# Kernel tuning notes

Hardware: AMD Instinct MI355X
Metric: run time of the kernel (lower is better)

Reference implementation:

```python
import jax, jax.numpy as jnp
from jax import lax
import numpy as np

DN = ('NCHW', 'OIHW', 'NCHW')


def _conv(x, w, b, stride, pad):
    y = lax.conv_general_dilated(x, w, (stride, stride), [(pad, pad), (pad, pad)],
                                 dimension_numbers=DN)
    return y + b[None, :, None, None]


def _conv_t(x, w, b):
    # torch ConvTranspose2d(k=4, stride=2, padding=1) equivalent:
    # lhs_dilation=2, effective padding k-1-p = 2 on each side -> output 2H x 2W
    y = lax.conv_general_dilated(x, w, (1, 1), [(2, 2), (2, 2)],
                                 lhs_dilation=(2, 2), dimension_numbers=DN)
    return y + b[None, :, None, None]


def setup_inputs() -> dict:
    key = jax.random.key(0)
    ks = jax.random.split(key, 16)
    D, K = 8, 512  # latent_dim, codebook_size

    def w(k, shape, fan_in):
        return jax.random.normal(k, shape, jnp.float32) * (1.0 / np.sqrt(fan_in))

    inp = {
        'x': jax.random.uniform(ks[0], (32, 3, 256, 256), jnp.float32),
        # encoder
        'enc_w1': w(ks[1], (32, 3, 4, 4), 3 * 16), 'enc_b1': jnp.zeros((32,), jnp.float32),
        'enc_w2': w(ks[2], (64, 32, 4, 4), 32 * 16), 'enc_b2': jnp.zeros((64,), jnp.float32),
        'enc_w3': w(ks[3], (D, 64, 1, 1), 64), 'enc_b3': jnp.zeros((D,), jnp.float32),
        # codebook, uniform(-1/K, 1/K) as in torch init
        'codebook': jax.random.uniform(ks[4], (K, D), jnp.float32, -1.0 / K, 1.0 / K),
        # decoder
        'dec_w1': w(ks[5], (64, D, 3, 3), D * 9), 'dec_b1': jnp.zeros((64,), jnp.float32),
        'dect_w1': w(ks[6], (64, 64, 4, 4), 64 * 16), 'dect_b1': jnp.zeros((64,), jnp.float32),
        'dect_w2': w(ks[7], (32, 64, 4, 4), 64 * 16), 'dect_b2': jnp.zeros((32,), jnp.float32),
        'dec_w2': w(ks[8], (3, 32, 3, 3), 32 * 9), 'dec_b2': jnp.zeros((3,), jnp.float32),
    }
    return inp


def reference(x, enc_w1, enc_b1, enc_w2, enc_b2, enc_w3, enc_b3, codebook,
              dec_w1, dec_b1, dect_w1, dect_b1, dect_w2, dect_b2, dec_w2, dec_b2):
    commitment_cost = 0.25
    B = x.shape[0]
    D = codebook.shape[1]

    # encoder
    h = jax.nn.relu(_conv(x, enc_w1, enc_b1, 2, 1))
    h = jax.nn.relu(_conv(h, enc_w2, enc_b2, 2, 1))
    z = _conv(h, enc_w3, enc_b3, 1, 0)                      # [B, D, H/4, W/4]

    # VQ: pairwise squared distances, argmin, gather
    z_flat = z.transpose(0, 2, 3, 1).reshape(-1, D)          # [N, D] in NHWC order
    distances = (jnp.sum(z_flat ** 2, axis=1, keepdims=True)
                 + jnp.sum(codebook ** 2, axis=1)
                 - 2.0 * z_flat @ codebook.T)                 # [N, K]
    encoding_indices = jnp.argmin(distances, axis=1)          # [N]
    # NOTE: faithful to original bug - reshaped directly into NCHW without permute
    z_q = codebook[encoding_indices].reshape(z.shape)

    commitment_loss = jnp.mean((z - lax.stop_gradient(z_q)) ** 2)
    codebook_loss = jnp.mean((z_q - lax.stop_gradient(z)) ** 2)
    vq_loss = codebook_loss + commitment_cost * commitment_loss

    # straight-through estimator
    z_q = z + lax.stop_gradient(z_q - z)

    # decoder
    h = jax.nn.relu(_conv(z_q, dec_w1, dec_b1, 1, 1))
    h = jax.nn.relu(_conv_t(h, dect_w1, dect_b1))
    h = jax.nn.relu(_conv_t(h, dect_w2, dect_b2))
    x_recon = jax.nn.sigmoid(_conv(h, dec_w2, dec_b2, 1, 1))

    return x_recon, vq_loss, encoding_indices.reshape(B, -1)
```

## Files before the change

### kernel.cpp

```cpp
#include <hip/hip_runtime.h>
#include <hip/hip_bf16.h>
#include <math.h>


__device__ __forceinline__ int rfl(int v) { return __builtin_amdgcn_readfirstlane(v); }

typedef __attribute__((ext_vector_type(8))) short s8v;
typedef __attribute__((ext_vector_type(4))) float f4v;

__device__ __forceinline__ ushort f2bf(float f) {
    __hip_bfloat16 h = __float2bfloat16(f);
    return *(ushort*)&h;
}

__global__ __launch_bounds__(256) void k_conv1(const float* __restrict__ x, const float* __restrict__ w,
                                               const float* __restrict__ bias, float* __restrict__ out) {
    int t = blockIdx.x * 256 + threadIdx.x;
    int ow  = t & 127;
    int oh0 = ((t >> 7) & 31) * 4;
    int co0 = rfl((t >> 12) & 3) * 8;
    int b   = rfl(t >> 14);
    float acc[4][8] = {};
    for (int ci = 0; ci < 3; ci++) {
        const float* xp = x + (b * 3 + ci) * 65536;
        const float* wp = w + (co0 * 3 + ci) * 16;
        #pragma unroll
        for (int r = 0; r < 10; r++) {
            int ih = oh0 * 2 - 1 + r;
            bool rok = (ih >= 0) && (ih < 256);
            int ihc = rok ? ih : 0;
            float v[4];
            #pragma unroll
            for (int c = 0; c < 4; c++) {
                int iw = ow * 2 - 1 + c;
                bool ok = rok && (iw >= 0) && (iw < 256);
                int iwc = iw < 0 ? 0 : (iw > 255 ? 255 : iw);
                float vv = xp[ihc * 256 + iwc];
                v[c] = ok ? vv : 0.f;
            }
            #pragma unroll
            for (int o = 0; o < 4; o++) {
                int kh = r - 2 * o;
                if (kh >= 0 && kh < 4) {
                    #pragma unroll
                    for (int cc = 0; cc < 8; cc++) {
                        const float* wc = wp + cc * 48 + kh * 4;
                        acc[o][cc] = __builtin_fmaf(v[0], wc[0], acc[o][cc]);
                        acc[o][cc] = __builtin_fmaf(v[1], wc[1], acc[o][cc]);
                        acc[o][cc] = __builtin_fmaf(v[2], wc[2], acc[o][cc]);
                        acc[o][cc] = __builtin_fmaf(v[3], wc[3], acc[o][cc]);
                    }
                }
            }
        }
    }
    #pragma unroll
    for (int cc = 0; cc < 8; cc++) {
        float bv = bias[co0 + cc];
        #pragma unroll
        for (int o = 0; o < 4; o++) {
            float v = acc[o][cc] + bv;
            out[((b * 32 + co0 + cc) * 128 + oh0 + o) * 128 + ow] = v > 0.f ? v : 0.f;
        }
    }
}

__global__ __launch_bounds__(256) void k_conv2t(const float* __restrict__ h1, const float* __restrict__ w,
                                                const float* __restrict__ bias, float* __restrict__ out) {
    __shared__ float P[16][18][2][10];
    int bx = blockIdx.x;
    int b  = bx >> 6;
    int ty = (bx >> 3) & 7, tx = bx & 7;
    int oh0 = ty * 8, ow0 = tx * 8;
    int tid = threadIdx.x;
    int lane = tid & 63;
    int dy = lane >> 3, dx = lane & 7;
    int co_base = rfl(tid >> 6) * 16;
    int oh = oh0 + dy, ow = ow0 + dx;
    float s00 = 0.f, s01 = 0.f, s02 = 0.f, s03 = 0.f;
    float s10 = 0.f, s11 = 0.f, s12 = 0.f, s13 = 0.f;
    float s20 = 0.f, s21 = 0.f, s22 = 0.f, s23 = 0.f;
    float s30 = 0.f, s31 = 0.f, s32 = 0.f, s33 = 0.f;

    #pragma unroll
    for (int pass = 0; pass < 2; pass++) {
        int cib = pass * 16;
        __syncthreads();
        for (int i = tid; i < 16 * 18 * 18; i += 256) {
            int cl = i / 324, rem = i - cl * 324;
            int r = rem / 18, c = rem - r * 18;
            int ih = oh0 * 2 - 1 + r, iw = ow0 * 2 - 1 + c;
            float v = 0.f;
            if (ih >= 0 && ih < 128 && iw >= 0 && iw < 128)
                v = h1[(b * 32 + cib + cl) * 16384 + ih * 128 + iw];
            P[cl][r][c & 1][c >> 1] = v;
        }
        __syncthreads();
        #pragma unroll
        for (int cc = 0; cc < 4; cc++) {
            int co0 = co_base + cc * 4;
            float a0 = (cc == 0) ? s00 : (cc == 1) ? s10 : (cc == 2) ? s20 : s30;
            float a1 = (cc == 0) ? s01 : (cc == 1) ? s11 : (cc == 2) ? s21 : s31;
            float a2 = (cc == 0) ? s02 : (cc == 1) ? s12 : (cc == 2) ? s22 : s32;
            float a3 = (cc == 0) ? s03 : (cc == 1) ? s13 : (cc == 2) ? s23 : s33;
            for (int cl = 0; cl < 16; cl++) {
                const float* wp0 = w + ((co0 + 0) * 32 + cib + cl) * 16;
                const float* wp1 = w + ((co0 + 1) * 32 + cib + cl) * 16;
                const float* wp2 = w + ((co0 + 2) * 32 + cib + cl) * 16;
                const float* wp3 = w + ((co0 + 3) * 32 + cib + cl) * 16;
                #pragma unroll
                for (int kh = 0; kh < 4; kh++) {
                    int r = 2 * dy + kh;
                    float v0 = P[cl][r][0][dx];
                    float v1 = P[cl][r][1][dx];
                    float v2 = P[cl][r][0][dx + 1];
                    float v3 = P[cl][r][1][dx + 1];
                    a0 = __builtin_fmaf(v0, wp0[kh*4+0], a0); a0 = __builtin_fmaf(v1, wp0[kh*4+1], a0);
                    a0 = __builtin_fmaf(v2, wp0[kh*4+2], a0); a0 = __builtin_fmaf(v3, wp0[kh*4+3], a0);
                    a1 = __builtin_fmaf(v0, wp1[kh*4+0], a1); a1 = __builtin_fmaf(v1, wp1[kh*4+1], a1);
                    a1 = __builtin_fmaf(v2, wp1[kh*4+2], a1); a1 = __builtin_fmaf(v3, wp1[kh*4+3], a1);
                    a2 = __builtin_fmaf(v0, wp2[kh*4+0], a2); a2 = __builtin_fmaf(v1, wp2[kh*4+1], a2);
                    a2 = __builtin_fmaf(v2, wp2[kh*4+2], a2); a2 = __builtin_fmaf(v3, wp2[kh*4+3], a2);
                    a3 = __builtin_fmaf(v0, wp3[kh*4+0], a3); a3 = __builtin_fmaf(v1, wp3[kh*4+1], a3);
                    a3 = __builtin_fmaf(v2, wp3[kh*4+2], a3); a3 = __builtin_fmaf(v3, wp3[kh*4+3], a3);
                }
            }
            if (cc == 0)      { s00 = a0; s01 = a1; s02 = a2; s03 = a3; }
            else if (cc == 1) { s10 = a0; s11 = a1; s12 = a2; s13 = a3; }
            else if (cc == 2) { s20 = a0; s21 = a1; s22 = a2; s23 = a3; }
            else              { s30 = a0; s31 = a1; s32 = a2; s33 = a3; }
        }
    }
    float r0, r1, r2, r3;
    #pragma unroll
    for (int cc = 0; cc < 4; cc++) {
        int co0 = co_base + cc * 4;
        if (cc == 0)      { r0 = s00; r1 = s01; r2 = s02; r3 = s03; }
        else if (cc == 1) { r0 = s10; r1 = s11; r2 = s12; r3 = s13; }
        else if (cc == 2) { r0 = s20; r1 = s21; r2 = s22; r3 = s23; }
        else              { r0 = s30; r1 = s31; r2 = s32; r3 = s33; }
        float v0 = r0 + bias[co0 + 0], v1 = r1 + bias[co0 + 1];
        float v2 = r2 + bias[co0 + 2], v3 = r3 + bias[co0 + 3];
        out[((b * 64 + co0 + 0) * 64 + oh) * 64 + ow] = v0 > 0.f ? v0 : 0.f;
        out[((b * 64 + co0 + 1) * 64 + oh) * 64 + ow] = v1 > 0.f ? v1 : 0.f;
        out[((b * 64 + co0 + 2) * 64 + oh) * 64 + ow] = v2 > 0.f ? v2 : 0.f;
        out[((b * 64 + co0 + 3) * 64 + oh) * 64 + ow] = v3 > 0.f ? v3 : 0.f;
    }
}

__global__ __launch_bounds__(256) void k_conv3(const float* __restrict__ h2, const float* __restrict__ w,
                                               const float* __restrict__ bias, float* __restrict__ zf) {
    __shared__ float wl[8][64];
    __shared__ float bl[8];
    int tid = threadIdx.x;
    for (int i = tid; i < 512; i += 256) wl[i >> 6][i & 63] = w[i];
    if (tid < 8) bl[tid] = bias[tid];
    __syncthreads();
    int t = blockIdx.x * 256 + tid;
    int b = t >> 12, hw = t & 4095;
    float acc[8];
    for (int d = 0; d < 8; d++) acc[d] = 0.f;
    for (int ci = 0; ci < 64; ci++) {
        float v = h2[(b * 64 + ci) * 4096 + hw];
        for (int d = 0; d < 8; d++) acc[d] = __builtin_fmaf(v, wl[d][ci], acc[d]);
    }
    for (int d = 0; d < 8; d++)
        zf[(b * 8 + d) * 4096 + hw] = acc[d] + bl[d];
}

__global__ __launch_bounds__(256) void k_vq(const float* __restrict__ zf, const float* __restrict__ cb,
                                            int* __restrict__ idx, float* __restrict__ out_idx) {
    __shared__ float cbs[512][8];
    __shared__ float c2s[512];
    int tid = threadIdx.x;
    for (int i = tid; i < 4096; i += 256) cbs[i >> 3][i & 7] = cb[i];
    __syncthreads();
    for (int k = tid; k < 512; k += 256) {
        float s = 0.f;
        for (int d = 0; d < 8; d++) {
            float c = cbs[k][d];
            s = s + __fmul_rn(c, c);
        }
        c2s[k] = s;
    }
    __syncthreads();
    int n = blockIdx.x * 256 + tid;
    int b = n >> 12, hw = n & 4095;
    float zv[8], s1 = 0.f;
    for (int d = 0; d < 8; d++) {
        float z = zf[(b * 8 + d) * 4096 + hw];
        zv[d] = z;
        s1 = s1 + __fmul_rn(z, z);
    }
    float best = 3.4e38f; int bi = 0;
    for (int k = 0; k < 512; k++) {
        float dot = 0.f;
        for (int d = 0; d < 8; d++) dot = __builtin_fmaf(zv[d], cbs[k][d], dot);
        float a = s1 + c2s[k];
        float dist = a - __fmul_rn(2.0f, dot);
        if (dist < best) { best = dist; bi = k; }
    }
    idx[n] = bi;
    out_idx[n] = (float)bi;
}

__global__ __launch_bounds__(256) void k_zq(const int* __restrict__ idx, const float* __restrict__ cb,
                                            const float* __restrict__ zf, float* __restrict__ zq,
                                            double* __restrict__ partial) {
    __shared__ double red[256];
    int t = blockIdx.x * 256 + threadIdx.x;
    float q = cb[idx[t >> 3] * 8 + (t & 7)];
    zq[t] = q;
    double d = (double)zf[t] - (double)q;
    red[threadIdx.x] = d * d;
    __syncthreads();
    for (int s = 128; s > 0; s >>= 1) {
        if (threadIdx.x < s) red[threadIdx.x] += red[threadIdx.x + s];
        __syncthreads();
    }
    if (threadIdx.x == 0) partial[blockIdx.x] = red[0];
}

__global__ __launch_bounds__(256) void k_loss_fin(const double* __restrict__ partial, float* __restrict__ out_loss) {
    __shared__ double red[256];
    double s = 0.0;
    for (int i = threadIdx.x; i < 4096; i += 256) s += partial[i];
    red[threadIdx.x] = s;
    __syncthreads();
    for (int st = 128; st > 0; st >>= 1) {
        if (threadIdx.x < st) red[threadIdx.x] += red[threadIdx.x + st];
        __syncthreads();
    }
    if (threadIdx.x == 0)
        out_loss[0] = (float)(1.25 * red[0] / 1048576.0);
}

__global__ __launch_bounds__(256) void k_dec1(const float* __restrict__ zq, const float* __restrict__ w,
                                              const float* __restrict__ bias, float* __restrict__ out) {
    int t = blockIdx.x * 256 + threadIdx.x;
    int ow  = t & 63;
    int oh0 = ((t >> 6) & 15) * 4;
    int co0 = rfl((t >> 10) & 7) * 8;
    int b   = rfl(t >> 13);
    float acc[4][8] = {};
    for (int ci = 0; ci < 8; ci++) {
        const float* ip = zq + (b * 8 + ci) * 4096;
        const float* wp = w + (co0 * 8 + ci) * 9;
        #pragma unroll
        for (int r = 0; r < 6; r++) {
            int ih = oh0 - 1 + r;
            bool rok = (ih >= 0) && (ih < 64);
            int ihc = rok ? ih : 0;
            float v[3];
            #pragma unroll
            for (int c = 0; c < 3; c++) {
                int iw = ow - 1 + c;
                bool ok = rok && (iw >= 0) && (iw < 64);
                int iwc = iw < 0 ? 0 : (iw > 63 ? 63 : iw);
                float vv = ip[ihc * 64 + iwc];
                v[c] = ok ? vv : 0.f;
            }
            #pragma unroll
            for (int o = 0; o < 4; o++) {
                int kh = r - o;
                if (kh >= 0 && kh < 3) {
                    #pragma unroll
                    for (int cc = 0; cc < 8; cc++) {
                        const float* wc = wp + cc * 72 + kh * 3;
                        acc[o][cc] = __builtin_fmaf(v[0], wc[0], acc[o][cc]);
                        acc[o][cc] = __builtin_fmaf(v[1], wc[1], acc[o][cc]);
                        acc[o][cc] = __builtin_fmaf(v[2], wc[2], acc[o][cc]);
                    }
                }
            }
        }
    }
    #pragma unroll
    for (int cc = 0; cc < 8; cc++) {
        float bv = bias[co0 + cc];
        #pragma unroll
        for (int o = 0; o < 4; o++) {
            float v = acc[o][cc] + bv;
            out[((b * 64 + co0 + cc) * 64 + oh0 + o) * 64 + ow] = v > 0.f ? v : 0.f;
        }
    }
}

template <int CI, int CO>
__global__ __launch_bounds__(256) void k_wprep(const float* __restrict__ w, ushort* __restrict__ Wf) {
    constexpr int NT = CO / 16;
    int t = blockIdx.x * 256 + threadIdx.x;
    if (t >= 4 * NT * 8 * 64) return;
    int lane = t & 63;
    int kt = (t >> 6) & 7;
    int nt = (t >> 9) % NT;
    int q  = t / (512 * NT);
    int py = q >> 1, px = q & 1;
    int n = nt * 16 + (lane & 15);
    int cb = (kt & 1) * 32 + (lane >> 4) * 8;
    int tap = kt >> 1, dy = tap >> 1, dx = tap & 1;
    #pragma unroll
    for (int jj = 0; jj < 8; jj++) {
        int ci = cb + jj;
        float v = w[((n * CI + ci) * 4 + (py + 2 * dy)) * 4 + (px + 2 * dx)];
        Wf[(((q * NT + nt) * 8 + kt) * 64 + lane) * 8 + jj] = f2bf(v);
    }
}

template <int CI, int CO, int HIN>
__global__ __launch_bounds__(256) void k_dect_mfma(const float* __restrict__ in, const ushort* __restrict__ Wf,
                                                   const float* __restrict__ bias, float* __restrict__ out) {
    constexpr int NT = CO / 16;
    constexpr int TILES = HIN / 16;
    constexpr int HOUT = 2 * HIN;
    __shared__ alignas(16) ushort L[18 * 18 * 72];
    int blk = blockIdx.x;
    int b = blk / (TILES * TILES);
    int tile = blk - b * (TILES * TILES);
    int i0 = (tile / TILES) * 16, j0 = (tile % TILES) * 16;
    const float* ip = in + (size_t)b * CI * HIN * HIN;
    for (int e = threadIdx.x; e < 18 * 18 * CI; e += 256) {
        int ci = e / 324; int rem = e - ci * 324;
        int row = rem / 18; int col = rem - row * 18;
        int ih = i0 - 1 + row, iw = j0 - 1 + col;
        float v = 0.f;
        if (ih >= 0 && ih < HIN && iw >= 0 && iw < HIN)
            v = ip[(size_t)ci * (HIN * HIN) + ih * HIN + iw];
        L[(row * 18 + col) * 72 + ci] = f2bf(v);
    }
    __syncthreads();
    int wv = threadIdx.x >> 6;
    int lane = threadIdx.x & 63;
    int py = wv >> 1, px = wv & 1;
    int m = lane & 15, quad = lane >> 4;
    const ushort* wq = Wf + (size_t)wv * NT * 8 * 64 * 8;
    for (int il = 0; il < 16; il++) {
        s8v a[8];
        #pragma unroll
        for (int kt = 0; kt < 8; kt++) {
            int tap = kt >> 1, dy = tap >> 1, dx = tap & 1;
            int r = il + py + dy, cl = m + px + dx;
            a[kt] = *(s8v*)&L[(r * 18 + cl) * 72 + (kt & 1) * 32 + quad * 8];
        }
        #pragma unroll
        for (int nt = 0; nt < NT; nt++) {
            f4v acc = {0.f, 0.f, 0.f, 0.f};
            #pragma unroll
            for (int kt = 0; kt < 8; kt++) {
                s8v bf = *(const s8v*)&wq[((nt * 8 + kt) * 64 + lane) * 8];
                acc = __builtin_amdgcn_mfma_f32_16x16x32_bf16(a[kt], bf, acc, 0, 0, 0);
            }
            int co = nt * 16 + m;
            float bv = bias[co];
            int y = 2 * (i0 + il) + py;
            #pragma unroll
            for (int reg = 0; reg < 4; reg++) {
                int jD = j0 + quad * 4 + reg;
                int xx = 2 * jD + px;
                float v = acc[reg] + bv;
                out[((size_t)(b * CO + co) * HOUT + y) * HOUT + xx] = v > 0.f ? v : 0.f;
            }
        }
    }
}

__global__ __launch_bounds__(256) void k_dec2(const float* __restrict__ in, const float* __restrict__ w,
                                              const float* __restrict__ bias, float* __restrict__ out) {
    int t = blockIdx.x * 256 + threadIdx.x;
    int x  = t & 255;
    int y0 = ((t >> 8) & 63) * 4;
    int b  = rfl(t >> 14);
    float acc[4][3] = {};
    for (int ci = 0; ci < 32; ci++) {
        const float* ip = in + (size_t)(b * 32 + ci) * 65536;
        const float* wp = w + ci * 9;
        #pragma unroll
        for (int rr = 0; rr < 6; rr++) {
            int ih = y0 - 1 + rr;
            bool rok = (ih >= 0) && (ih < 256);
            int ihc = rok ? ih : 0;
            float v[3];
            #pragma unroll
            for (int c = 0; c < 3; c++) {
                int iw = x - 1 + c;
                bool ok = rok && (iw >= 0) && (iw < 256);
                int iwc = iw < 0 ? 0 : (iw > 255 ? 255 : iw);
                float vv = ip[ihc * 256 + iwc];
                v[c] = ok ? vv : 0.f;
            }
            #pragma unroll
            for (int o = 0; o < 4; o++) {
                int kh = rr - o;
                if (kh >= 0 && kh < 3) {
                    #pragma unroll
                    for (int co = 0; co < 3; co++) {
                        const float* wc = wp + co * 288 + kh * 3;
                        acc[o][co] = __builtin_fmaf(v[0], wc[0], acc[o][co]);
                        acc[o][co] = __builtin_fmaf(v[1], wc[1], acc[o][co]);
                        acc[o][co] = __builtin_fmaf(v[2], wc[2], acc[o][co]);
                    }
                }
            }
        }
    }
    #pragma unroll
    for (int co = 0; co < 3; co++) {
        float bv = bias[co];
        #pragma unroll
        for (int o = 0; o < 4; o++) {
            float v = acc[o][co] + bv;
            out[((size_t)(b * 3 + co) * 256 + y0 + o) * 256 + x] = 1.0f / (1.0f + expf(-v));
        }
    }
}

extern "C" void kernel_launch(void* const* d_in, const int* in_sizes, int n_in,
                              void* d_out, int out_size, void* d_ws, size_t ws_size,
                              hipStream_t stream) {
    const float* x    = (const float*)d_in[0];
    const float* ew1  = (const float*)d_in[1];
    const float* eb1  = (const float*)d_in[2];
    const float* ew2  = (const float*)d_in[3];
    const float* eb2  = (const float*)d_in[4];
    const float* ew3  = (const float*)d_in[5];
    const float* eb3  = (const float*)d_in[6];
    const float* cb   = (const float*)d_in[7];
    const float* dw1  = (const float*)d_in[8];
    const float* db1  = (const float*)d_in[9];
    const float* dtw1 = (const float*)d_in[10];
    const float* dtb1 = (const float*)d_in[11];
    const float* dtw2 = (const float*)d_in[12];
    const float* dtb2 = (const float*)d_in[13];
    const float* dw2  = (const float*)d_in[14];
    const float* db2  = (const float*)d_in[15];

    char* ws = (char*)d_ws;
    float*  z32  = (float*) (ws);
    float*  zq   = (float*) (ws + 4194304);
    int*    idx  = (int*)   (ws + 8388608);
    double* part = (double*)(ws + 8912896);
    ushort* Wf1  = (ushort*)(ws + 8945664);
    ushort* Wf2  = (ushort*)(ws + 9076736);
    char* region = ws + 9142272;

    size_t fixed = 9142272;
    size_t avail = (ws_size > fixed) ? ws_size - fixed : 0;
    int ce = 32, cd = 32;
    while (ce > 1 && (size_t)ce * 3145728ull > avail) ce >>= 1;
    while (cd > 1 && (size_t)cd * 13631488ull > avail) cd >>= 1;

    float* h1c = (float*)region;
    float* h2c = (float*)(region + (size_t)ce * 2097152ull);
    float* d3c = (float*) region;
    float* d4c = (float*) (region + (size_t)cd * 1048576ull);
    float* d5c = (float*) (region + (size_t)cd * 5242880ull);

    float* out      = (float*)d_out;
    float* out_loss = out + 6291456;
    float* out_idx  = out + 6291457;

    for (int c = 0; c < 32 / ce; c++) {
        const float* xc = x + (size_t)c * ce * 196608ull;
        k_conv1<<<ce * 64, 256, 0, stream>>>(xc, ew1, eb1, h1c);
        k_conv2t<<<ce * 64, 256, 0, stream>>>(h1c, ew2, eb2, h2c);
        k_conv3<<<ce * 16,  256, 0, stream>>>(h2c, ew3, eb3, z32 + (size_t)c * ce * 32768ull);
    }

    k_vq<<<512, 256, 0, stream>>>(z32, cb, idx, out_idx);
    k_zq<<<4096, 256, 0, stream>>>(idx, cb, z32, zq, part);
    k_loss_fin<<<1, 256, 0, stream>>>(part, out_loss);

    k_wprep<64, 64><<<32, 256, 0, stream>>>(dtw1, Wf1);
    k_wprep<64, 32><<<16, 256, 0, stream>>>(dtw2, Wf2);

    for (int c = 0; c < 32 / cd; c++) {
        const float* zqc = zq + (size_t)c * cd * 32768ull;
        float* outc = out + (size_t)c * cd * 196608ull;
        k_dec1<<<cd * 32, 256, 0, stream>>>(zqc, dw1, db1, d3c);
        k_dect_mfma<64, 64, 64 ><<<cd * 16, 256, 0, stream>>>(d3c, Wf1, dtb1, d4c);
        k_dect_mfma<64, 32, 128><<<cd * 64, 256, 0, stream>>>(d4c, Wf2, dtb2, d5c);
        k_dec2<<<cd * 64, 256, 0, stream>>>(d5c, dw2, db2, outc);
    }
}
```

Baseline: 982.7 us.

## Store decoder intermediates in bf16, halve deconv tiles, and register-prefetch conv2 inputs

Decoder intermediates (dec1, both transposed-conv outputs) are now stored as bf16 instead of fp32. This halves their global memory traffic and removes the per-element conversion at LDS staging in the MFMA kernels. The MFMA deconv tiles shrink from 16x16 to 8x16, doubling the block count and cutting LDS use. The encoder conv2 kernel now processes 8 input channels per pass and prefetches the next slab into registers so global loads overlap compute. The cost is extra precision loss from rounding intermediates to bf16, plus more barriers and passes in conv2.

```diff
diff --git a/kernel.cpp b/kernel.cpp
--- a/kernel.cpp
+++ b/kernel.cpp
@@ -11,6 +11,9 @@
 __device__ __forceinline__ ushort f2bf(float f) {
     __hip_bfloat16 h = __float2bfloat16(f);
     return *(ushort*)&h;
+}
+__device__ __forceinline__ float bf2f(ushort u) {
+    return __uint_as_float(((unsigned int)u) << 16);
 }
 
 __global__ __launch_bounds__(256) void k_conv1(const float* __restrict__ x, const float* __restrict__ w,
@@ -67,7 +70,7 @@
 
 __global__ __launch_bounds__(256) void k_conv2t(const float* __restrict__ h1, const float* __restrict__ w,
                                                 const float* __restrict__ bias, float* __restrict__ out) {
-    __shared__ float P[16][18][2][10];
+    __shared__ float P[8][18][2][10];
     int bx = blockIdx.x;
     int b  = bx >> 6;
     int ty = (bx >> 3) & 7, tx = bx & 7;
@@ -81,21 +84,49 @@
     float s10 = 0.f, s11 = 0.f, s12 = 0.f, s13 = 0.f;
     float s20 = 0.f, s21 = 0.f, s22 = 0.f, s23 = 0.f;
     float s30 = 0.f, s31 = 0.f, s32 = 0.f, s33 = 0.f;
-
+    float pf[11];
     #pragma unroll
-    for (int pass = 0; pass < 2; pass++) {
-        int cib = pass * 16;
-        __syncthreads();
-        for (int i = tid; i < 16 * 18 * 18; i += 256) {
+    for (int k = 0; k < 11; k++) {
+        int i = tid + (k << 8);
+        float v = 0.f;
+        if (i < 2592) {
             int cl = i / 324, rem = i - cl * 324;
             int r = rem / 18, c = rem - r * 18;
             int ih = oh0 * 2 - 1 + r, iw = ow0 * 2 - 1 + c;
-            float v = 0.f;
             if (ih >= 0 && ih < 128 && iw >= 0 && iw < 128)
-                v = h1[(b * 32 + cib + cl) * 16384 + ih * 128 + iw];
-            P[cl][r][c & 1][c >> 1] = v;
-        }
+                v = h1[(b * 32 + cl) * 16384 + ih * 128 + iw];
+        }
+        pf[k] = v;
+    }
+    for (int pass = 0; pass < 4; pass++) {
         __syncthreads();
+        #pragma unroll
+        for (int k = 0; k < 11; k++) {
+            int i = tid + (k << 8);
+            if (i < 2592) {
+                int cl = i / 324, rem = i - cl * 324;
+                int r = rem / 18, c = rem - r * 18;
+                P[cl][r][c & 1][c >> 1] = pf[k];
+            }
+        }
+        __syncthreads();
+        if (pass < 3) {
+            int cib = (pass + 1) * 8;
+            #pragma unroll
+            for (int k = 0; k < 11; k++) {
+                int i = tid + (k << 8);
+                float v = 0.f;
+                if (i < 2592) {
+                    int cl = i / 324, rem = i - cl * 324;
+                    int r = rem / 18, c = rem - r * 18;
+                    int ih = oh0 * 2 - 1 + r, iw = ow0 * 2 - 1 + c;
+                    if (ih >= 0 && ih < 128 && iw >= 0 && iw < 128)
+                        v = h1[(b * 32 + cib + cl) * 16384 + ih * 128 + iw];
+                }
+                pf[k] = v;
+            }
+        }
+        int cib = pass * 8;
         #pragma unroll
         for (int cc = 0; cc < 4; cc++) {
             int co0 = co_base + cc * 4;
@@ -103,7 +134,7 @@
             float a1 = (cc == 0) ? s01 : (cc == 1) ? s11 : (cc == 2) ? s21 : s31;
             float a2 = (cc == 0) ? s02 : (cc == 1) ? s12 : (cc == 2) ? s22 : s32;
             float a3 = (cc == 0) ? s03 : (cc == 1) ? s13 : (cc == 2) ? s23 : s33;
-            for (int cl = 0; cl < 16; cl++) {
+            for (int cl = 0; cl < 8; cl++) {
                 const float* wp0 = w + ((co0 + 0) * 32 + cib + cl) * 16;
                 const float* wp1 = w + ((co0 + 1) * 32 + cib + cl) * 16;
                 const float* wp2 = w + ((co0 + 2) * 32 + cib + cl) * 16;
@@ -236,7 +267,7 @@
 }
 
 __global__ __launch_bounds__(256) void k_dec1(const float* __restrict__ zq, const float* __restrict__ w,
-                                              const float* __restrict__ bias, float* __restrict__ out) {
+                                              const float* __restrict__ bias, ushort* __restrict__ out) {
     int t = blockIdx.x * 256 + threadIdx.x;
     int ow  = t & 63;
     int oh0 = ((t >> 6) & 15) * 4;
@@ -281,7 +312,7 @@
         #pragma unroll
         for (int o = 0; o < 4; o++) {
             float v = acc[o][cc] + bv;
-            out[((b * 64 + co0 + cc) * 64 + oh0 + o) * 64 + ow] = v > 0.f ? v : 0.f;
+            out[((b * 64 + co0 + cc) * 64 + oh0 + o) * 64 + ow] = f2bf(v > 0.f ? v : 0.f);
         }
     }
 }
@@ -308,25 +339,27 @@
 }
 
 template <int CI, int CO, int HIN>
-__global__ __launch_bounds__(256) void k_dect_mfma(const float* __restrict__ in, const ushort* __restrict__ Wf,
-                                                   const float* __restrict__ bias, float* __restrict__ out) {
+__global__ __launch_bounds__(256) void k_dect_mfma(const ushort* __restrict__ in, const ushort* __restrict__ Wf,
+                                                   const float* __restrict__ bias, ushort* __restrict__ out) {
     constexpr int NT = CO / 16;
-    constexpr int TILES = HIN / 16;
+    constexpr int TX = HIN / 16;
+    constexpr int TY = HIN / 8;
     constexpr int HOUT = 2 * HIN;
-    __shared__ alignas(16) ushort L[18 * 18 * 72];
+    __shared__ alignas(16) ushort L[10 * 18 * 72];
     int blk = blockIdx.x;
-    int b = blk / (TILES * TILES);
-    int tile = blk - b * (TILES * TILES);
-    int i0 = (tile / TILES) * 16, j0 = (tile % TILES) * 16;
-    const float* ip = in + (size_t)b * CI * HIN * HIN;
-    for (int e = threadIdx.x; e < 18 * 18 * CI; e += 256) {
-        int ci = e / 324; int rem = e - ci * 324;
+    int b = blk / (TY * TX);
+    int tile = blk - b * (TY * TX);
+    int tyy = tile / TX, txx = tile - tyy * TX;
+    int i0 = tyy * 8, j0 = txx * 16;
+    const ushort* ip = in + (size_t)b * CI * HIN * HIN;
+    for (int e = threadIdx.x; e < 10 * 18 * CI; e += 256) {
+        int ci = e / 180; int rem = e - ci * 180;
         int row = rem / 18; int col = rem - row * 18;
         int ih = i0 - 1 + row, iw = j0 - 1 + col;
-        float v = 0.f;
+        ushort v = 0;
         if (ih >= 0 && ih < HIN && iw >= 0 && iw < HIN)
             v = ip[(size_t)ci * (HIN * HIN) + ih * HIN + iw];
-        L[(row * 18 + col) * 72 + ci] = f2bf(v);
+        L[(row * 18 + col) * 72 + ci] = v;
     }
     __syncthreads();
     int wv = threadIdx.x >> 6;
@@ -334,7 +367,7 @@
     int py = wv >> 1, px = wv & 1;
     int m = lane & 15, quad = lane >> 4;
     const ushort* wq = Wf + (size_t)wv * NT * 8 * 64 * 8;
-    for (int il = 0; il < 16; il++) {
+    for (int il = 0; il < 8; il++) {
         s8v a[8];
         #pragma unroll
         for (int kt = 0; kt < 8; kt++) {
@@ -358,13 +391,13 @@
                 int jD = j0 + quad * 4 + reg;
                 int xx = 2 * jD + px;
                 float v = acc[reg] + bv;
-                out[((size_t)(b * CO + co) * HOUT + y) * HOUT + xx] = v > 0.f ? v : 0.f;
-            }
-        }
-    }
-}
-
-__global__ __launch_bounds__(256) void k_dec2(const float* __restrict__ in, const float* __restrict__ w,
+                out[((size_t)(b * CO + co) * HOUT + y) * HOUT + xx] = f2bf(v > 0.f ? v : 0.f);
+            }
+        }
+    }
+}
+
+__global__ __launch_bounds__(256) void k_dec2(const ushort* __restrict__ in, const float* __restrict__ w,
                                               const float* __restrict__ bias, float* __restrict__ out) {
     int t = blockIdx.x * 256 + threadIdx.x;
     int x  = t & 255;
@@ -372,7 +405,7 @@
     int b  = rfl(t >> 14);
     float acc[4][3] = {};
     for (int ci = 0; ci < 32; ci++) {
-        const float* ip = in + (size_t)(b * 32 + ci) * 65536;
+        const ushort* ip = in + (size_t)(b * 32 + ci) * 65536;
         const float* wp = w + ci * 9;
         #pragma unroll
         for (int rr = 0; rr < 6; rr++) {
@@ -385,7 +418,7 @@
                 int iw = x - 1 + c;
                 bool ok = rok && (iw >= 0) && (iw < 256);
                 int iwc = iw < 0 ? 0 : (iw > 255 ? 255 : iw);
-                float vv = ip[ihc * 256 + iwc];
+                float vv = bf2f(ip[ihc * 256 + iwc]);
                 v[c] = ok ? vv : 0.f;
             }
             #pragma unroll
@@ -447,13 +480,13 @@
     size_t avail = (ws_size > fixed) ? ws_size - fixed : 0;
     int ce = 32, cd = 32;
     while (ce > 1 && (size_t)ce * 3145728ull > avail) ce >>= 1;
-    while (cd > 1 && (size_t)cd * 13631488ull > avail) cd >>= 1;
-
-    float* h1c = (float*)region;
-    float* h2c = (float*)(region + (size_t)ce * 2097152ull);
-    float* d3c = (float*) region;
-    float* d4c = (float*) (region + (size_t)cd * 1048576ull);
-    float* d5c = (float*) (region + (size_t)cd * 5242880ull);
+    while (cd > 1 && (size_t)cd * 6815744ull > avail) cd >>= 1;
+
+    float*  h1c = (float*)region;
+    float*  h2c = (float*)(region + (size_t)ce * 2097152ull);
+    ushort* d3c = (ushort*)region;
+    ushort* d4c = (ushort*)(region + (size_t)cd * 524288ull);
+    ushort* d5c = (ushort*)(region + (size_t)cd * 2621440ull);
 
     float* out      = (float*)d_out;
     float* out_loss = out + 6291456;
@@ -477,8 +510,8 @@
         const float* zqc = zq + (size_t)c * cd * 32768ull;
         float* outc = out + (size_t)c * cd * 196608ull;
         k_dec1<<<cd * 32, 256, 0, stream>>>(zqc, dw1, db1, d3c);
-        k_dect_mfma<64, 64, 64 ><<<cd * 16, 256, 0, stream>>>(d3c, Wf1, dtb1, d4c);
-        k_dect_mfma<64, 32, 128><<<cd * 64, 256, 0, stream>>>(d4c, Wf2, dtb2, d5c);
+        k_dect_mfma<64, 64, 64 ><<<cd * 32, 256, 0, stream>>>(d3c, Wf1, dtb1, d4c);
+        k_dect_mfma<64, 32, 128><<<cd * 128, 256, 0, stream>>>(d4c, Wf2, dtb2, d5c);
         k_dec2<<<cd * 64, 256, 0, stream>>>(d5c, dw2, db2, outc);
     }
 }
```

Measured after the change: 1.019 ms. 3.7% more time.
